# Kernel tuning notes

Measured on AMD Instinct MI355X. Metric: run time of the kernel, lower is better.

Reference implementation:

```python
import jax, jax.numpy as jnp
import numpy as np
from jax import lax

L, H, NUM_CONVS, KSIZE = 8192, 128, 4, 7
EPS = 1e-5


def _pos_encoding(length, dim, dtype):
    pos = jnp.arange(length, dtype=jnp.float32)[:, None]
    i = jnp.arange(dim, dtype=jnp.float32)[None, :]
    angle = pos / jnp.power(10000.0, (2.0 * jnp.floor(i / 2.0)) / dim)
    pe = jnp.where((jnp.arange(dim) % 2 == 0)[None, :], jnp.sin(angle), jnp.cos(angle))
    return pe.astype(dtype)


def _layer_norm(x):
    mu = jnp.mean(x, axis=-1, keepdims=True)
    var = jnp.mean(jnp.square(x - mu), axis=-1, keepdims=True)
    return (x - mu) * lax.rsqrt(var + EPS)


def _conv1d_same(x, w, b):
    # x: [L, H]; w: [H_out, H_in, K]; b: [H_out]. SAME padding over sequence.
    lhs = x.T[None]  # [1, H, L]
    out = lax.conv_general_dilated(lhs, w, window_strides=(1,), padding='SAME',
                                   dimension_numbers=('NCH', 'OIH', 'NCH'))
    return (out[0] + b[:, None]).T  # [L, H]


def setup_inputs() -> dict:
    key = jax.random.key(0)
    ks = jax.random.split(key, 12)
    s = 0.02
    return {
        'x': jax.random.normal(ks[0], (L, H), jnp.float32),
        'conv_w': jax.random.normal(ks[1], (NUM_CONVS, H, H, KSIZE), jnp.float32) * s,
        'conv_b': jax.random.normal(ks[2], (NUM_CONVS, H), jnp.float32) * s,
        'Wq': jax.random.normal(ks[3], (H, H), jnp.float32) * s,
        'bq': jax.random.normal(ks[4], (H,), jnp.float32) * s,
        'Wk': jax.random.normal(ks[5], (H, H), jnp.float32) * s,
        'bk': jax.random.normal(ks[6], (H,), jnp.float32) * s,
        'Wv': jax.random.normal(ks[7], (H, H), jnp.float32) * s,
        'bv': jax.random.normal(ks[8], (H,), jnp.float32) * s,
        'Wff': jax.random.normal(ks[9], (H, H), jnp.float32) * s,
        'bff': jax.random.normal(ks[10], (H,), jnp.float32) * s,
    }


def reference(x, conv_w, conv_b, Wq, bq, Wk, bk, Wv, bv, Wff, bff):
    h = x + _pos_encoding(x.shape[0], x.shape[1], x.dtype)
    # conv stack: LN -> conv -> residual, repeated num_convs times
    for i in range(NUM_CONVS):
        residual = h
        h = _conv1d_same(_layer_norm(h), conv_w[i], conv_b[i]) + residual
    # self-attention (single-head as written in the source)
    residual = h
    n = _layer_norm(h)
    q = n @ Wq.T + bq
    k = n @ Wk.T + bk
    v = n @ Wv.T + bv
    scale = 1.0 / jnp.sqrt(jnp.asarray(H, h.dtype))
    attn = jax.nn.softmax((q @ k.T) * scale, axis=-1)  # [L, L]
    h = attn @ v + residual
    # feed-forward
    residual = h
    h = jax.nn.relu(_layer_norm(h) @ Wff.T + bff) + residual
    return h
```

## Files before the change

### kernel.cpp

```cpp
#include <hip/hip_runtime.h>

#define LL 8192
#define HH 128

typedef __attribute__((ext_vector_type(8))) short short8v;
typedef __attribute__((ext_vector_type(4))) short short4v;
typedef __attribute__((ext_vector_type(4))) float f32x4;

__device__ inline short f2bf(float f) {
    union { float f; unsigned u; } x; x.f = f;
    unsigned r = (x.u + 0x7fffu + ((x.u >> 16) & 1u)) >> 16;
    return (short)r;
}
__device__ inline float bf2f(short s) {
    union { unsigned u; float f; } x; x.u = ((unsigned)(unsigned short)s) << 16;
    return x.f;
}

__device__ inline unsigned ln_pack(const float* rowF, int lane) {
    float2 xv = *(const float2*)&rowF[lane * 2];
    float s = xv.x + xv.y, s2 = xv.x * xv.x + xv.y * xv.y;
#pragma unroll
    for (int off = 32; off >= 1; off >>= 1) {
        s  += __shfl_xor(s,  off, 64);
        s2 += __shfl_xor(s2, off, 64);
    }
    float mu = s * (1.f / 128.f);
    float var = s2 * (1.f / 128.f) - mu * mu;
    float rstd = rsqrtf(var + 1e-5f);
    unsigned lo = (unsigned short)f2bf((xv.x - mu) * rstd);
    unsigned hi = (unsigned short)f2bf((xv.y - mu) * rstd);
    return lo | (hi << 16);
}

__global__ __launch_bounds__(256) void repack_all(const float* __restrict__ w,
                                                  const float* __restrict__ Wq,
                                                  const float* __restrict__ Wk,
                                                  const float* __restrict__ Wv,
                                                  const float* __restrict__ bq,
                                                  const float* __restrict__ bk,
                                                  const float* __restrict__ bv,
                                                  const float* __restrict__ Wff,
                                                  short* __restrict__ wkb,
                                                  short* __restrict__ wqkvb,
                                                  float* __restrict__ b3,
                                                  short* __restrict__ wffb) {
    const float qs = 0.08838834764831845f;
    int idx = blockIdx.x * 256 + threadIdx.x;
    if (idx < 458752) {
        int k = idx % 7;
        int t = idx / 7;
        int i = t % HH; t /= HH;
        int o = t % HH;
        int lay = t / HH;
        wkb[((lay * 7 + k) * HH + o) * HH + i] = f2bf(w[idx]);
    } else {
        int j = idx - 458752;
        if (j < 49152) {
            int t = j >> 14, r = j & 16383;
            float v = (t == 0) ? Wq[r] * qs : (t == 1) ? Wk[r] : Wv[r];
            wqkvb[j] = f2bf(v);
        } else if (j < 49536) {
            int jj = j - 49152;
            b3[jj] = (jj < 128) ? bq[jj] * qs : (jj < 256) ? bk[jj - 128] : bv[jj - 256];
        } else if (j < 65920) {
            int jj = j - 49536;
            wffb[jj] = f2bf(Wff[jj]);
        }
    }
}

__global__ __launch_bounds__(256) void conv4qkv_kernel(const float* __restrict__ x,
                                                       const short* __restrict__ wkb,
                                                       const float* __restrict__ conv_b,
                                                       const short* __restrict__ wqkvb,
                                                       const float* __restrict__ b3,
                                                       float* __restrict__ hB,
                                                       short* __restrict__ qb,
                                                       short* __restrict__ kb,
                                                       short* __restrict__ vt) {
    __shared__ float sF[48][132];
    __shared__ short sA[54][136];
    __shared__ short sT[4][32][17];
    int tid = threadIdx.x;
    int w = tid >> 6, lane = tid & 63;
    int l15 = lane & 15, quad = lane >> 4;
    int m0 = blockIdx.x * 16;
    int c0 = w * 32;

    for (int idx = tid; idx < 48 * 32; idx += 256) {
        int r = idx >> 5, c4 = (idx & 31) << 2;
        int g = m0 - 16 + r;
        float4 val = make_float4(0.f, 0.f, 0.f, 0.f);
        if (g >= 0 && g < LL) {
            val = *(const float4*)&x[g * HH + c4];
#pragma unroll
            for (int j = 0; j < 4; j++) {
                int i = c4 + j;
                float e = (float)(i & ~1) / 128.f;
                float ang = (float)g / powf(10000.f, e);
                float pe = (i & 1) ? cosf(ang) : sinf(ang);
                ((float*)&val)[j] += pe;
            }
        }
        *(float4*)&sF[r][c4] = val;
    }
    for (int idx = tid; idx < 6 * 68; idx += 256) {
        int rr = idx / 68, cc = idx % 68;
        int row = (rr < 3) ? rr : 48 + rr;
        ((unsigned*)&sA[row][0])[cc] = 0u;
    }

    for (int lay = 0; lay < 4; lay++) {
        __syncthreads();
#pragma unroll
        for (int rr = 0; rr < 12; rr++) {
            int row = rr * 4 + w;
            int g = m0 - 16 + row;
            unsigned packed = ln_pack(&sF[row][0], lane);
            if (g < 0 || g >= LL) packed = 0u;
            ((unsigned*)&sA[row + 3][0])[lane] = packed;
        }
        __syncthreads();
        f32x4 acc[3][2];
#pragma unroll
        for (int mt = 0; mt < 3; mt++) { acc[mt][0] = (f32x4)(0.f); acc[mt][1] = (f32x4)(0.f); }
        const short* wl = wkb + lay * 7 * HH * HH;
        for (int k = 0; k < 7; k++) {
            const short* b0 = wl + (k * HH + c0 + l15) * HH;
            const short* b1 = b0 + 16 * HH;
#pragma unroll
            for (int ks = 0; ks < 4; ks++) {
                short8v bf0 = *(const short8v*)&b0[ks * 32 + quad * 8];
                short8v bf1 = *(const short8v*)&b1[ks * 32 + quad * 8];
#pragma unroll
                for (int mt = 0; mt < 3; mt++) {
                    short8v af = *(const short8v*)&sA[mt * 16 + l15 + k][ks * 32 + quad * 8];
                    acc[mt][0] = __builtin_amdgcn_mfma_f32_16x16x32_bf16(af, bf0, acc[mt][0], 0, 0, 0);
                    acc[mt][1] = __builtin_amdgcn_mfma_f32_16x16x32_bf16(af, bf1, acc[mt][1], 0, 0, 0);
                }
            }
        }
        float bb0 = conv_b[lay * HH + c0 + l15], bb1 = conv_b[lay * HH + c0 + 16 + l15];
#pragma unroll
        for (int mt = 0; mt < 3; mt++)
#pragma unroll
            for (int r = 0; r < 4; r++) {
                int row = mt * 16 + quad * 4 + r;
                sF[row][c0 + l15]      += acc[mt][0][r] + bb0;
                sF[row][c0 + 16 + l15] += acc[mt][1][r] + bb1;
            }
    }
    __syncthreads();
    for (int idx = tid; idx < 16 * 32; idx += 256) {
        int r = idx >> 5, c4 = (idx & 31) << 2;
        *(float4*)&hB[(m0 + r) * HH + c4] = *(const float4*)&sF[16 + r][c4];
    }
#pragma unroll
    for (int rr = 0; rr < 4; rr++) {
        int row = rr * 4 + w;
        ((unsigned*)&sA[row][0])[lane] = ln_pack(&sF[16 + row][0], lane);
    }
    __syncthreads();
    short8v af4[4];
#pragma unroll
    for (int ks = 0; ks < 4; ks++)
        af4[ks] = *(const short8v*)&sA[l15][ks * 32 + quad * 8];

    for (int t = 0; t < 3; t++) {
        f32x4 acc0 = (f32x4)(0.f), acc1 = (f32x4)(0.f);
        const short* b0 = wqkvb + (t * 128 + c0 + l15) * HH;
        const short* b1 = b0 + 16 * HH;
#pragma unroll
        for (int ks = 0; ks < 4; ks++) {
            short8v bf0 = *(const short8v*)&b0[ks * 32 + quad * 8];
            short8v bf1 = *(const short8v*)&b1[ks * 32 + quad * 8];
            acc0 = __builtin_amdgcn_mfma_f32_16x16x32_bf16(af4[ks], bf0, acc0, 0, 0, 0);
            acc1 = __builtin_amdgcn_mfma_f32_16x16x32_bf16(af4[ks], bf1, acc1, 0, 0, 0);
        }
        float bb0 = b3[t * 128 + c0 + l15], bb1 = b3[t * 128 + c0 + 16 + l15];
        if (t < 2) {
            short* o = (t == 0) ? qb : kb;
#pragma unroll
            for (int r = 0; r < 4; r++) {
                int lr = m0 + quad * 4 + r;
                o[lr * HH + c0 + l15]      = f2bf(acc0[r] + bb0);
                o[lr * HH + c0 + 16 + l15] = f2bf(acc1[r] + bb1);
            }
        } else {
#pragma unroll
            for (int r = 0; r < 4; r++) {
                sT[w][l15][quad * 4 + r]      = f2bf(acc0[r] + bb0);
                sT[w][16 + l15][quad * 4 + r] = f2bf(acc1[r] + bb1);
            }
            asm volatile("s_waitcnt lgkmcnt(0)" ::: "memory");
#pragma unroll
            for (int cc = 0; cc < 8; cc++) {
                int col = cc * 4 + quad;
                vt[(c0 + col) * LL + m0 + l15] = sT[w][col][l15];
            }
        }
    }
}

#define FBN 64

__global__ __launch_bounds__(256, 2) void flash_mfma_kernel(const short* __restrict__ qs,
                                                            const short* __restrict__ ksrc,
                                                            const short* __restrict__ vsrc,
                                                            short* __restrict__ PO,
                                                            float* __restrict__ Pl,
                                                            int segrows) {
    __shared__ short sK[16 * 64 * 8];
    __shared__ short sV[16 * 64 * 8];
    __shared__ short sP[4][32][72];

    const int tid = threadIdx.x;
    const int w = tid >> 6, lane = tid & 63;
    const int l15 = lane & 15, quad = lane >> 4;
    const int m0 = blockIdx.x * 128;
    const int seg = blockIdx.y;
    const int jbeg = seg * segrows;
    const int nchunk = segrows >> 6;

    const int vdt_base = (w >> 1);
    const int vks2 = w & 1;

    short8v qf[2][4];
#pragma unroll
    for (int mt = 0; mt < 2; mt++)
#pragma unroll
        for (int ks = 0; ks < 4; ks++)
            qf[mt][ks] = *(const short8v*)&qs[(m0 + w * 32 + mt * 16 + l15) * HH + ks * 32 + quad * 8];

    float l_r[2][4] = {{0.f, 0.f, 0.f, 0.f}, {0.f, 0.f, 0.f, 0.f}};
    f32x4 o_acc[2][8];
#pragma unroll
    for (int mt = 0; mt < 2; mt++)
#pragma unroll
        for (int dt = 0; dt < 8; dt++) o_acc[mt][dt] = (f32x4)(0.f);

    short8v kr[4], vr[4];
#pragma unroll
    for (int r = 0; r < 4; r++) {
        kr[r] = *(const short8v*)&ksrc[(jbeg + r * 16 + l15) * HH + w * 32 + quad * 8];
        vr[r] = *(const short8v*)&vsrc[((2 * r + vdt_base) * 16 + l15) * LL + jbeg + vks2 * 32 + quad * 8];
    }

    for (int c = 0; c < nchunk; c++) {
        __syncthreads();
#pragma unroll
        for (int r = 0; r < 4; r++) {
            *(short8v*)&sK[((w + 4 * r) * 64 + lane) * 8] = kr[r];
            *(short8v*)&sV[((w + 4 * r) * 64 + lane) * 8] = vr[r];
        }
        __syncthreads();
        if (c + 1 < nchunk) {
            const int j1 = jbeg + (c + 1) * FBN;
#pragma unroll
            for (int r = 0; r < 4; r++) {
                kr[r] = *(const short8v*)&ksrc[(j1 + r * 16 + l15) * HH + w * 32 + quad * 8];
                vr[r] = *(const short8v*)&vsrc[((2 * r + vdt_base) * 16 + l15) * LL + j1 + vks2 * 32 + quad * 8];
            }
        }
        f32x4 s_acc[2][4];
#pragma unroll
        for (int mt = 0; mt < 2; mt++)
#pragma unroll
            for (int nt = 0; nt < 4; nt++) s_acc[mt][nt] = (f32x4)(0.f);
#pragma unroll
        for (int nt = 0; nt < 4; nt++)
#pragma unroll
            for (int ks = 0; ks < 4; ks++) {
                short8v kf = *(const short8v*)&sK[((nt * 4 + ks) * 64 + lane) * 8];
                s_acc[0][nt] = __builtin_amdgcn_mfma_f32_16x16x32_bf16(qf[0][ks], kf, s_acc[0][nt], 0, 0, 0);
                s_acc[1][nt] = __builtin_amdgcn_mfma_f32_16x16x32_bf16(qf[1][ks], kf, s_acc[1][nt], 0, 0, 0);
            }
#pragma unroll
        for (int mt = 0; mt < 2; mt++)
#pragma unroll
            for (int nt = 0; nt < 4; nt++)
#pragma unroll
                for (int r = 0; r < 4; r++) {
                    float p = __expf(fminf(s_acc[mt][nt][r], 30.f));
                    l_r[mt][r] += p;
                    union { float f; unsigned u; } cv; cv.f = p;
                    sP[w][mt * 16 + quad * 4 + r][nt * 16 + l15] = (short)(cv.u >> 16);
                }
        asm volatile("s_waitcnt lgkmcnt(0)" ::: "memory");
#pragma unroll
        for (int ks2 = 0; ks2 < 2; ks2++) {
            short8v pf0 = *(const short8v*)&sP[w][l15][ks2 * 32 + quad * 8];
            short8v pf1 = *(const short8v*)&sP[w][16 + l15][ks2 * 32 + quad * 8];
#pragma unroll
            for (int dt = 0; dt < 8; dt++) {
                short8v vf = *(const short8v*)&sV[((dt * 2 + ks2) * 64 + lane) * 8];
                o_acc[0][dt] = __builtin_amdgcn_mfma_f32_16x16x32_bf16(pf0, vf, o_acc[0][dt], 0, 0, 0);
                o_acc[1][dt] = __builtin_amdgcn_mfma_f32_16x16x32_bf16(pf1, vf, o_acc[1][dt], 0, 0, 0);
            }
        }
    }
#pragma unroll
    for (int mt = 0; mt < 2; mt++)
#pragma unroll
        for (int r = 0; r < 4; r++) {
            float v = l_r[mt][r];
            v += __shfl_xor(v, 1, 64);
            v += __shfl_xor(v, 2, 64);
            v += __shfl_xor(v, 4, 64);
            v += __shfl_xor(v, 8, 64);
            if (l15 == 0)
                Pl[seg * LL + m0 + w * 32 + mt * 16 + quad * 4 + r] = v;
        }
#pragma unroll
    for (int mt = 0; mt < 2; mt++)
#pragma unroll
        for (int dt = 0; dt < 8; dt++)
#pragma unroll
            for (int r = 0; r < 4; r++)
                PO[(size_t)seg * LL * HH + (m0 + w * 32 + mt * 16 + quad * 4 + r) * HH + dt * 16 + l15] =
                    f2bf(o_acc[mt][dt][r]);
}

__global__ __launch_bounds__(256) void ff_kernel(const float* __restrict__ hin,
                                                 const short* __restrict__ PO,
                                                 const float* __restrict__ Pl,
                                                 const short* __restrict__ wffb,
                                                 const float* __restrict__ bff,
                                                 float* __restrict__ out,
                                                 int nsplit) {
    __shared__ float sF[16][132];
    __shared__ short sA[16][136];
    __shared__ float sLi[16];
    int tid = threadIdx.x;
    int w = tid >> 6, lane = tid & 63;
    int l15 = lane & 15, quad = lane >> 4;
    int m0 = blockIdx.x * 16;

    if (tid < 16) {
        float s = 0.f;
        for (int seg = 0; seg < nsplit; seg++) s += Pl[seg * LL + m0 + tid];
        sLi[tid] = 1.f / s;
    }
    __syncthreads();
    for (int idx = tid; idx < 16 * 32; idx += 256) {
        int r = idx >> 5, c4 = (idx & 31) << 2;
        float4 hv = *(const float4*)&hin[(m0 + r) * HH + c4];
        float s0 = 0.f, s1 = 0.f, s2 = 0.f, s3 = 0.f;
        for (int seg = 0; seg < nsplit; seg++) {
            short4v pv = *(const short4v*)&PO[(size_t)seg * LL * HH + (m0 + r) * HH + c4];
            s0 += bf2f(pv[0]); s1 += bf2f(pv[1]); s2 += bf2f(pv[2]); s3 += bf2f(pv[3]);
        }
        float li = sLi[r];
        *(float4*)&sF[r][c4] = make_float4(hv.x + s0 * li, hv.y + s1 * li,
                                           hv.z + s2 * li, hv.w + s3 * li);
    }
    __syncthreads();
#pragma unroll
    for (int rr = 0; rr < 4; rr++) {
        int row = rr * 4 + w;
        ((unsigned*)&sA[row][0])[lane] = ln_pack(&sF[row][0], lane);
    }
    __syncthreads();
    int c0 = w * 32;
    f32x4 acc0 = (f32x4)(0.f), acc1 = (f32x4)(0.f);
    const short* b0 = wffb + (c0 + l15) * HH;
    const short* b1 = b0 + 16 * HH;
#pragma unroll
    for (int ks = 0; ks < 4; ks++) {
        short8v af = *(const short8v*)&sA[l15][ks * 32 + quad * 8];
        short8v bf0 = *(const short8v*)&b0[ks * 32 + quad * 8];
        short8v bf1 = *(const short8v*)&b1[ks * 32 + quad * 8];
        acc0 = __builtin_amdgcn_mfma_f32_16x16x32_bf16(af, bf0, acc0, 0, 0, 0);
        acc1 = __builtin_amdgcn_mfma_f32_16x16x32_bf16(af, bf1, acc1, 0, 0, 0);
    }
    float bb0 = bff[c0 + l15], bb1 = bff[c0 + 16 + l15];
#pragma unroll
    for (int r = 0; r < 4; r++) {
        int lr = quad * 4 + r;
        out[(m0 + lr) * HH + c0 + l15]      = fmaxf(acc0[r] + bb0, 0.f) + sF[lr][c0 + l15];
        out[(m0 + lr) * HH + c0 + 16 + l15] = fmaxf(acc1[r] + bb1, 0.f) + sF[lr][c0 + 16 + l15];
    }
}

extern "C" void kernel_launch(void* const* d_in, const int* in_sizes, int n_in,
                              void* d_out, int out_size, void* d_ws, size_t ws_size,
                              hipStream_t stream) {
    const float* x      = (const float*)d_in[0];
    const float* conv_w = (const float*)d_in[1];
    const float* conv_b = (const float*)d_in[2];
    const float* Wq = (const float*)d_in[3];
    const float* bq = (const float*)d_in[4];
    const float* Wk = (const float*)d_in[5];
    const float* bk = (const float*)d_in[6];
    const float* Wv = (const float*)d_in[7];
    const float* bv = (const float*)d_in[8];
    const float* Wff = (const float*)d_in[9];
    const float* bff = (const float*)d_in[10];
    float* out = (float*)d_out;

    char* ws = (char*)d_ws;
    const size_t MB = 1u << 20;
    float* hB   = (float*)(ws);
    short* qb   = (short*)(ws + 4 * MB);
    short* kb   = (short*)(ws + 6 * MB);
    short* vt   = (short*)(ws + 8 * MB);
    float* Pl   = (float*)(ws + 10 * MB);
    short* wffb = (short*)(ws + 10 * MB + 524288);
    short* PO   = (short*)(ws + 10 * MB + 524288 + 32768);
    short* wkb   = (short*)(ws + 16 * MB);
    short* wqkvb = (short*)(ws + 17 * MB);
    float* b3    = (float*)(ws + 17 * MB + 131072);

    int nsplit = (ws_size >= (size_t)44 * MB) ? 16 : 8;
    int segrows = LL / nsplit;

    repack_all<<<2050, 256, 0, stream>>>(conv_w, Wq, Wk, Wv, bq, bk, bv, Wff,
                                         wkb, wqkvb, b3, wffb);
    conv4qkv_kernel<<<LL / 16, 256, 0, stream>>>(x, wkb, conv_b, wqkvb, b3,
                                                 hB, qb, kb, vt);
    flash_mfma_kernel<<<dim3(LL / 128, nsplit), 256, 0, stream>>>(qb, kb, vt, PO, Pl, segrows);
    ff_kernel<<<LL / 16, 256, 0, stream>>>(hB, PO, Pl, wffb, bff, out, nsplit);
}
```

Baseline: 216.1 us.

## Precompute positional encoding once, swizzle LDS A-tile, vectorize layernorm packing

Positional encoding is now added once per row in the repack kernel and written to a workspace buffer. Previously the conv kernel recomputed it for each 48-row halo tile, so every row was evaluated about three times with powf/sin/cos. The LDS A-tile drops its padded stride in favour of an XOR swizzle, which shrinks shared memory, and the transpose scratch now aliases sA. Layernorm packing moves to 8 elements per lane with a 16-lane reduction and adds a launch-bounds occupancy hint. The trade is an extra global write and read of the full hidden state.

```diff
diff --git a/kernel.cpp b/kernel.cpp
--- a/kernel.cpp
+++ b/kernel.cpp
@@ -17,23 +17,40 @@
     return x.f;
 }
 
-__device__ inline unsigned ln_pack(const float* rowF, int lane) {
-    float2 xv = *(const float2*)&rowF[lane * 2];
-    float s = xv.x + xv.y, s2 = xv.x * xv.x + xv.y * xv.y;
-#pragma unroll
-    for (int off = 32; off >= 1; off >>= 1) {
+__device__ inline short* sAp(short* base, int row, int col) {
+    int byte = (row << 8) + (col << 1);
+    byte ^= (row & 7) << 4;
+    return (short*)((char*)base + byte);
+}
+
+__device__ inline short8v ln_pack8(const float* rowF, int l15) {
+    const float4 a = *(const float4*)&rowF[l15 * 8];
+    const float4 b = *(const float4*)&rowF[l15 * 8 + 4];
+    float s  = (a.x + a.y) + (a.z + a.w) + (b.x + b.y) + (b.z + b.w);
+    float s2 = a.x * a.x + a.y * a.y + a.z * a.z + a.w * a.w
+             + b.x * b.x + b.y * b.y + b.z * b.z + b.w * b.w;
+#pragma unroll
+    for (int off = 1; off <= 8; off <<= 1) {
         s  += __shfl_xor(s,  off, 64);
         s2 += __shfl_xor(s2, off, 64);
     }
     float mu = s * (1.f / 128.f);
     float var = s2 * (1.f / 128.f) - mu * mu;
     float rstd = rsqrtf(var + 1e-5f);
-    unsigned lo = (unsigned short)f2bf((xv.x - mu) * rstd);
-    unsigned hi = (unsigned short)f2bf((xv.y - mu) * rstd);
-    return lo | (hi << 16);
-}
-
-__global__ __launch_bounds__(256) void repack_all(const float* __restrict__ w,
+    short8v r;
+    r[0] = f2bf((a.x - mu) * rstd);
+    r[1] = f2bf((a.y - mu) * rstd);
+    r[2] = f2bf((a.z - mu) * rstd);
+    r[3] = f2bf((a.w - mu) * rstd);
+    r[4] = f2bf((b.x - mu) * rstd);
+    r[5] = f2bf((b.y - mu) * rstd);
+    r[6] = f2bf((b.z - mu) * rstd);
+    r[7] = f2bf((b.w - mu) * rstd);
+    return r;
+}
+
+__global__ __launch_bounds__(256) void repack_all(const float* __restrict__ x,
+                                                  const float* __restrict__ w,
                                                   const float* __restrict__ Wq,
                                                   const float* __restrict__ Wk,
                                                   const float* __restrict__ Wv,
@@ -44,7 +61,8 @@
                                                   short* __restrict__ wkb,
                                                   short* __restrict__ wqkvb,
                                                   float* __restrict__ b3,
-                                                  short* __restrict__ wffb) {
+                                                  short* __restrict__ wffb,
+                                                  float* __restrict__ h0) {
     const float qs = 0.08838834764831845f;
     int idx = blockIdx.x * 256 + threadIdx.x;
     if (idx < 458752) {
@@ -66,22 +84,38 @@
         } else if (j < 65920) {
             int jj = j - 49536;
             wffb[jj] = f2bf(Wff[jj]);
-        }
-    }
-}
-
-__global__ __launch_bounds__(256) void conv4qkv_kernel(const float* __restrict__ x,
-                                                       const short* __restrict__ wkb,
-                                                       const float* __restrict__ conv_b,
-                                                       const short* __restrict__ wqkvb,
-                                                       const float* __restrict__ b3,
-                                                       float* __restrict__ hB,
-                                                       short* __restrict__ qb,
-                                                       short* __restrict__ kb,
-                                                       short* __restrict__ vt) {
+        } else {
+            int p = j - 65920;
+            if (p < 262144) {
+                int g = p >> 5, c4 = (p & 31) << 2;
+                float4 val = *(const float4*)&x[g * HH + c4];
+                float fg = (float)g;
+#pragma unroll
+                for (int h = 0; h < 2; h++) {
+                    int i0 = c4 + h * 2;
+                    float e = (float)i0 / 128.f;
+                    float ang = fg / powf(10000.f, e);
+                    ((float*)&val)[h * 2]     += sinf(ang);
+                    ((float*)&val)[h * 2 + 1] += cosf(ang);
+                }
+                *(float4*)&h0[g * HH + c4] = val;
+            }
+        }
+    }
+}
+
+__global__ __launch_bounds__(256, 4) void conv4qkv_kernel(const float* __restrict__ h0,
+                                                          const short* __restrict__ wkb,
+                                                          const float* __restrict__ conv_b,
+                                                          const short* __restrict__ wqkvb,
+                                                          const float* __restrict__ b3,
+                                                          float* __restrict__ hB,
+                                                          short* __restrict__ qb,
+                                                          short* __restrict__ kb,
+                                                          short* __restrict__ vt) {
     __shared__ float sF[48][132];
-    __shared__ short sA[54][136];
-    __shared__ short sT[4][32][17];
+    __shared__ short sA[54 * 128];
+    short* sT = sA + 20 * 128;
     int tid = threadIdx.x;
     int w = tid >> 6, lane = tid & 63;
     int l15 = lane & 15, quad = lane >> 4;
@@ -92,34 +126,24 @@
         int r = idx >> 5, c4 = (idx & 31) << 2;
         int g = m0 - 16 + r;
         float4 val = make_float4(0.f, 0.f, 0.f, 0.f);
-        if (g >= 0 && g < LL) {
-            val = *(const float4*)&x[g * HH + c4];
-#pragma unroll
-            for (int j = 0; j < 4; j++) {
-                int i = c4 + j;
-                float e = (float)(i & ~1) / 128.f;
-                float ang = (float)g / powf(10000.f, e);
-                float pe = (i & 1) ? cosf(ang) : sinf(ang);
-                ((float*)&val)[j] += pe;
-            }
-        }
+        if (g >= 0 && g < LL) val = *(const float4*)&h0[g * HH + c4];
         *(float4*)&sF[r][c4] = val;
     }
-    for (int idx = tid; idx < 6 * 68; idx += 256) {
-        int rr = idx / 68, cc = idx % 68;
+    for (int idx = tid; idx < 6 * 64; idx += 256) {
+        int rr = idx >> 6, cc = idx & 63;
         int row = (rr < 3) ? rr : 48 + rr;
-        ((unsigned*)&sA[row][0])[cc] = 0u;
+        ((unsigned*)sA)[row * 64 + cc] = 0u;
     }
 
     for (int lay = 0; lay < 4; lay++) {
         __syncthreads();
 #pragma unroll
-        for (int rr = 0; rr < 12; rr++) {
-            int row = rr * 4 + w;
+        for (int rr = 0; rr < 3; rr++) {
+            int row = rr * 16 + w * 4 + quad;
+            short8v pk = ln_pack8(&sF[row][0], l15);
             int g = m0 - 16 + row;
-            unsigned packed = ln_pack(&sF[row][0], lane);
-            if (g < 0 || g >= LL) packed = 0u;
-            ((unsigned*)&sA[row + 3][0])[lane] = packed;
+            if (g < 0 || g >= LL) pk = (short8v)(short)0;
+            *(short8v*)sAp(sA, row + 3, l15 * 8) = pk;
         }
         __syncthreads();
         f32x4 acc[3][2];
@@ -135,7 +159,7 @@
                 short8v bf1 = *(const short8v*)&b1[ks * 32 + quad * 8];
 #pragma unroll
                 for (int mt = 0; mt < 3; mt++) {
-                    short8v af = *(const short8v*)&sA[mt * 16 + l15 + k][ks * 32 + quad * 8];
+                    short8v af = *(const short8v*)sAp(sA, mt * 16 + l15 + k, ks * 32 + quad * 8);
                     acc[mt][0] = __builtin_amdgcn_mfma_f32_16x16x32_bf16(af, bf0, acc[mt][0], 0, 0, 0);
                     acc[mt][1] = __builtin_amdgcn_mfma_f32_16x16x32_bf16(af, bf1, acc[mt][1], 0, 0, 0);
                 }
@@ -156,16 +180,15 @@
         int r = idx >> 5, c4 = (idx & 31) << 2;
         *(float4*)&hB[(m0 + r) * HH + c4] = *(const float4*)&sF[16 + r][c4];
     }
-#pragma unroll
-    for (int rr = 0; rr < 4; rr++) {
-        int row = rr * 4 + w;
-        ((unsigned*)&sA[row][0])[lane] = ln_pack(&sF[16 + row][0], lane);
+    {
+        int row = w * 4 + quad;
+        *(short8v*)sAp(sA, row, l15 * 8) = ln_pack8(&sF[16 + row][0], l15);
     }
     __syncthreads();
     short8v af4[4];
 #pragma unroll
     for (int ks = 0; ks < 4; ks++)
-        af4[ks] = *(const short8v*)&sA[l15][ks * 32 + quad * 8];
+        af4[ks] = *(const short8v*)sAp(sA, l15, ks * 32 + quad * 8);
 
     for (int t = 0; t < 3; t++) {
         f32x4 acc0 = (f32x4)(0.f), acc1 = (f32x4)(0.f);
@@ -190,14 +213,14 @@
         } else {
 #pragma unroll
             for (int r = 0; r < 4; r++) {
-                sT[w][l15][quad * 4 + r]      = f2bf(acc0[r] + bb0);
-                sT[w][16 + l15][quad * 4 + r] = f2bf(acc1[r] + bb1);
+                sT[(w * 32 + l15) * 17 + quad * 4 + r]      = f2bf(acc0[r] + bb0);
+                sT[(w * 32 + 16 + l15) * 17 + quad * 4 + r] = f2bf(acc1[r] + bb1);
             }
             asm volatile("s_waitcnt lgkmcnt(0)" ::: "memory");
 #pragma unroll
             for (int cc = 0; cc < 8; cc++) {
                 int col = cc * 4 + quad;
-                vt[(c0 + col) * LL + m0 + l15] = sT[w][col][l15];
+                vt[(c0 + col) * LL + m0 + l15] = sT[(w * 32 + col) * 17 + l15];
             }
         }
     }
@@ -330,7 +353,7 @@
                                                  float* __restrict__ out,
                                                  int nsplit) {
     __shared__ float sF[16][132];
-    __shared__ short sA[16][136];
+    __shared__ short sA[16 * 128];
     __shared__ float sLi[16];
     int tid = threadIdx.x;
     int w = tid >> 6, lane = tid & 63;
@@ -356,10 +379,9 @@
                                            hv.z + s2 * li, hv.w + s3 * li);
     }
     __syncthreads();
-#pragma unroll
-    for (int rr = 0; rr < 4; rr++) {
-        int row = rr * 4 + w;
-        ((unsigned*)&sA[row][0])[lane] = ln_pack(&sF[row][0], lane);
+    {
+        int row = w * 4 + quad;
+        *(short8v*)sAp(sA, row, l15 * 8) = ln_pack8(&sF[row][0], l15);
     }
     __syncthreads();
     int c0 = w * 32;
@@ -368,7 +390,7 @@
     const short* b1 = b0 + 16 * HH;
 #pragma unroll
     for (int ks = 0; ks < 4; ks++) {
-        short8v af = *(const short8v*)&sA[l15][ks * 32 + quad * 8];
+        short8v af = *(const short8v*)sAp(sA, l15, ks * 32 + quad * 8);
         short8v bf0 = *(const short8v*)&b0[ks * 32 + quad * 8];
         short8v bf1 = *(const short8v*)&b1[ks * 32 + quad * 8];
         acc0 = __builtin_amdgcn_mfma_f32_16x16x32_bf16(af, bf0, acc0, 0, 0, 0);
@@ -411,13 +433,14 @@
     short* wkb   = (short*)(ws + 16 * MB);
     short* wqkvb = (short*)(ws + 17 * MB);
     float* b3    = (float*)(ws + 17 * MB + 131072);
+    float* h0    = (float*)(ws + 18 * MB);
 
     int nsplit = (ws_size >= (size_t)44 * MB) ? 16 : 8;
     int segrows = LL / nsplit;
 
-    repack_all<<<2050, 256, 0, stream>>>(conv_w, Wq, Wk, Wv, bq, bk, bv, Wff,
-                                         wkb, wqkvb, b3, wffb);
-    conv4qkv_kernel<<<LL / 16, 256, 0, stream>>>(x, wkb, conv_b, wqkvb, b3,
+    repack_all<<<3074, 256, 0, stream>>>(x, conv_w, Wq, Wk, Wv, bq, bk, bv, Wff,
+                                         wkb, wqkvb, b3, wffb, h0);
+    conv4qkv_kernel<<<LL / 16, 256, 0, stream>>>(h0, wkb, conv_b, wqkvb, b3,
                                                  hB, qb, kb, vt);
     flash_mfma_kernel<<<dim3(LL / 128, nsplit), 256, 0, stream>>>(qb, kb, vt, PO, Pl, segrows);
     ff_kernel<<<LL / 16, 256, 0, stream>>>(hB, PO, Pl, wffb, bff, out, nsplit);
```

Result: slower. 224.4 us (+3.8%).
